# Performance work log

Hardware: AMD Instinct MI355X
Metric: run time of the kernel (lower is better)

## Reference

```python
import jax, jax.numpy as jnp
import numpy as np

N = 50000      # nodes
E = 800000     # edges (avg degree 16)
IN_DIM = 128
HID = 64       # num_hidden
HEADS = 1
NUM_LAYERS = 3       # -> 4 SNATConv layers total
SLOPE = 0.2          # negative_slope
THR = 0.01           # threhold: edges with attention < THR are pruned after layer 0


def setup_inputs() -> dict:
    key = jax.random.key(0)
    ks = jax.random.split(key, 16)
    s = 0.05
    x = jax.random.normal(ks[0], (N, IN_DIM), jnp.float32)
    edge_src = jax.random.randint(ks[1], (E,), 0, N)
    edge_dst = jax.random.randint(ks[2], (E,), 0, N)
    W_embed = jax.random.normal(ks[3], (IN_DIM, HID), jnp.float32) * s
    n_conv = NUM_LAYERS + 1
    # all conv layers map HID*HEADS -> HEADS*HID (heads==1 so square)
    W_gat = jax.random.normal(ks[4], (n_conv, HID, HEADS * HID), jnp.float32) * s
    a_l = jax.random.normal(ks[5], (n_conv, HEADS, HID), jnp.float32) * s
    a_r = jax.random.normal(ks[6], (n_conv, HEADS, HID), jnp.float32) * s
    d_cat = (NUM_LAYERS + 1) * HID
    W0 = jax.random.normal(ks[7], (d_cat, HID), jnp.float32) * s
    b0 = jnp.zeros((HID,), jnp.float32)
    W1 = jax.random.normal(ks[8], (HID, HID), jnp.float32) * s
    b1 = jnp.zeros((HID,), jnp.float32)
    W2 = jax.random.normal(ks[9], (HID, 1), jnp.float32) * s
    b2 = jnp.zeros((1,), jnp.float32)
    return {"x": x, "edge_src": edge_src, "edge_dst": edge_dst,
            "W_embed": W_embed, "W_gat": W_gat, "a_l": a_l, "a_r": a_r,
            "W0": W0, "b0": b0, "W1": W1, "b1": b1, "W2": W2, "b2": b2}


def _edge_softmax(e, dst):
    # e: [E, H] raw scores; softmax over incoming edges of each dst node
    m = jax.ops.segment_max(e, dst, num_segments=N)       # [N, H]
    a = jnp.exp(e - m[dst])
    s = jax.ops.segment_sum(a, dst, num_segments=N)       # [N, H]
    return a / jnp.maximum(s[dst], 1e-9)


def _snat_conv(h, W, al, ar, src, dst, mask):
    # h: [N, F_in]; W: [F_in, H*HID]; al/ar: [H, HID]
    feat = (h @ W).reshape(N, HEADS, HID)                 # [N, H, HID]
    el = jnp.sum(feat * al, axis=-1)                      # [N, H]
    er = jnp.sum(feat * ar, axis=-1)
    e = jax.nn.leaky_relu(el[src] + er[dst], SLOPE)       # [E, H]
    if mask is not None:
        e = jnp.where(mask, e, -1e9)                      # prune thresholded edges
    alpha = _edge_softmax(e, dst)                         # [E, H]
    out = jax.ops.segment_sum(feat[src] * alpha[..., None], dst, num_segments=N)
    return jax.nn.elu(out), alpha                         # [N, H, HID], [E, H]


def reference(x, edge_src, edge_dst, W_embed, W_gat, a_l, a_r, W0, b0, W1, b1, W2, b2):
    src, dst = edge_src, edge_dst
    h = jnp.tanh(x @ W_embed)                             # [N, HID]
    # layer 0: computes attention and the threshold mask (index_1 / index_0)
    h0, alpha = _snat_conv(h, W_gat[0], a_l[0], a_r[0], src, dst, None)
    mask = alpha >= THR                                   # [E, H] kept-edge mask
    h = h0.reshape(N, HEADS * HID)
    H_cat = [h]
    for l in range(1, NUM_LAYERS):                        # middle layers reuse mask
        hl, _ = _snat_conv(h, W_gat[l], a_l[l], a_r[l], src, dst, mask)
        h = hl.reshape(N, HEADS * HID)
        H_cat.append(h)
    feats, _ = _snat_conv(h, W_gat[NUM_LAYERS], a_l[NUM_LAYERS], a_r[NUM_LAYERS], src, dst, mask)
    feats = feats.mean(axis=1)                            # [N, HID] mean over heads
    f = jnp.concatenate(H_cat + [feats], axis=1)          # [N, (L+1)*HID]
    out = jax.nn.relu(f @ W0 + b0)                        # activationP
    out = jax.nn.relu(out @ W1 + b1)
    out = jax.nn.relu(out @ W2 + b2)                      # final F.relu
    return out                                            # [N, 1]
```

## Files before the change

### kernel.cpp

```cpp
#include <hip/hip_runtime.h>
#include <math.h>


#define CAP 80

__global__ void k_zero(int* __restrict__ counts, int N) {
  int i = blockIdx.x * 256 + threadIdx.x;
  if (i < N) counts[i] = 0;
}

__global__ void k_scatter2(const int* __restrict__ src, const int* __restrict__ dst,
                           int* __restrict__ counts, int* __restrict__ csr_src,
                           int E) {
  int e = blockIdx.x * blockDim.x + threadIdx.x;
  if (e < E) {
    int d = dst[e];
    int pos = atomicAdd(&counts[d], 1);
    if (pos < CAP) csr_src[d * CAP + pos] = src[e];
  }
}

#define SWS 68

#define STAGE_W(DST, SRC)                                            \
  {                                                                  \
    int k_ = threadIdx.x >> 2, p_ = threadIdx.x & 3;                 \
    const float* s_ = (SRC) + k_ * 64 + p_ * 16;                     \
    float* d_ = (DST) + k_ * SWS + p_ * 16;                          \
    _Pragma("unroll")                                                \
    for (int c_ = 0; c_ < 4; c_++)                                   \
      *(float4*)(d_ + c_ * 4) = *(const float4*)(s_ + c_ * 4);       \
  }

#define GEMM64(ACC, ABASE, ASTRIDE, KOFF)                            \
  { _Pragma("unroll 4")                                              \
    for (int k_ = 0; k_ < 64; k_++) {                                \
      float4 w4_ = *(const float4*)&sW[k_ * SWS + fq];               \
      float a0_ = (ABASE)[(nr +  0) * (ASTRIDE) + (KOFF) + k_];      \
      float a1_ = (ABASE)[(nr + 16) * (ASTRIDE) + (KOFF) + k_];      \
      float a2_ = (ABASE)[(nr + 32) * (ASTRIDE) + (KOFF) + k_];      \
      float a3_ = (ABASE)[(nr + 48) * (ASTRIDE) + (KOFF) + k_];      \
      ACC[0][0] = fmaf(a0_, w4_.x, ACC[0][0]);                       \
      ACC[0][1] = fmaf(a0_, w4_.y, ACC[0][1]);                       \
      ACC[0][2] = fmaf(a0_, w4_.z, ACC[0][2]);                       \
      ACC[0][3] = fmaf(a0_, w4_.w, ACC[0][3]);                       \
      ACC[1][0] = fmaf(a1_, w4_.x, ACC[1][0]);                       \
      ACC[1][1] = fmaf(a1_, w4_.y, ACC[1][1]);                       \
      ACC[1][2] = fmaf(a1_, w4_.z, ACC[1][2]);                       \
      ACC[1][3] = fmaf(a1_, w4_.w, ACC[1][3]);                       \
      ACC[2][0] = fmaf(a2_, w4_.x, ACC[2][0]);                       \
      ACC[2][1] = fmaf(a2_, w4_.y, ACC[2][1]);                       \
      ACC[2][2] = fmaf(a2_, w4_.z, ACC[2][2]);                       \
      ACC[2][3] = fmaf(a2_, w4_.w, ACC[2][3]);                       \
      ACC[3][0] = fmaf(a3_, w4_.x, ACC[3][0]);                       \
      ACC[3][1] = fmaf(a3_, w4_.y, ACC[3][1]);                       \
      ACC[3][2] = fmaf(a3_, w4_.z, ACC[3][2]);                       \
      ACC[3][3] = fmaf(a3_, w4_.w, ACC[3][3]);                       \
    } }

__global__ __launch_bounds__(256, 3) void k_embed_feat(
    const float* __restrict__ x, const float* __restrict__ We,
    const float* __restrict__ Wg, const float* __restrict__ al,
    const float* __restrict__ ar, float* __restrict__ feat,
    float* __restrict__ el, float* __restrict__ er, int N) {
  __shared__ float sA[64 * 129];
  __shared__ float sW[64 * SWS];
  __shared__ float sE[64 * 8];
  int tid = threadIdx.x, lane = tid & 63, wv = tid >> 6;
  int nb0 = blockIdx.x * 64, nl = N - 1;
  int r = tid >> 2, p = tid & 3;
  int nr = lane >> 2, fc = lane & 3;
  int fq = wv * 16 + fc * 4;
  {
    const float* gp = x + (size_t)min(nb0 + r, nl) * 128;
    #pragma unroll
    for (int half = 0; half < 2; half++) {
      const float* g = gp + half * 64 + p * 16;
      float4 v0 = *(const float4*)(g + 0), v1 = *(const float4*)(g + 4);
      float4 v2 = *(const float4*)(g + 8), v3 = *(const float4*)(g + 12);
      float* dp = &sA[r * 129 + half * 64 + p * 16];
      dp[0]=v0.x; dp[1]=v0.y; dp[2]=v0.z; dp[3]=v0.w;
      dp[4]=v1.x; dp[5]=v1.y; dp[6]=v1.z; dp[7]=v1.w;
      dp[8]=v2.x; dp[9]=v2.y; dp[10]=v2.z; dp[11]=v2.w;
      dp[12]=v3.x; dp[13]=v3.y; dp[14]=v3.z; dp[15]=v3.w;
    }
  }
  STAGE_W(sW, We);
  __syncthreads();
  float acc[4][4];
  #pragma unroll
  for (int m = 0; m < 4; m++)
    #pragma unroll
    for (int j = 0; j < 4; j++) acc[m][j] = 0.f;
  GEMM64(acc, sA, 129, 0);
  __syncthreads();
  STAGE_W(sW, We + 4096);
  __syncthreads();
  GEMM64(acc, sA, 129, 64);
  __syncthreads();
  STAGE_W(sW, Wg);
  #pragma unroll
  for (int m = 0; m < 4; m++)
    #pragma unroll
    for (int j = 0; j < 4; j++)
      sA[(nr + 16 * m) * 65 + fq + j] = tanhf(acc[m][j]);
  __syncthreads();
  float acc2[4][4];
  #pragma unroll
  for (int m = 0; m < 4; m++)
    #pragma unroll
    for (int j = 0; j < 4; j++) acc2[m][j] = 0.f;
  GEMM64(acc2, sA, 65, 0);
  {
    float alv[4], arv[4];
    *(float4*)&alv[0] = *(const float4*)(al + fq);
    *(float4*)&arv[0] = *(const float4*)(ar + fq);
    #pragma unroll
    for (int m = 0; m < 4; m++) {
      float pl = 0.f, pr = 0.f;
      #pragma unroll
      for (int j = 0; j < 4; j++) {
        pl = fmaf(acc2[m][j], alv[j], pl);
        pr = fmaf(acc2[m][j], arv[j], pr);
      }
      pl += __shfl_xor(pl, 1, 64); pl += __shfl_xor(pl, 2, 64);
      pr += __shfl_xor(pr, 1, 64); pr += __shfl_xor(pr, 2, 64);
      if (fc == 0) {
        sE[(nr + 16 * m) * 8 + wv] = pl;
        sE[(nr + 16 * m) * 8 + 4 + wv] = pr;
      }
    }
  }
  __syncthreads();
  #pragma unroll
  for (int m = 0; m < 4; m++)
    #pragma unroll
    for (int j = 0; j < 4; j++)
      sA[(nr + 16 * m) * 65 + fq + j] = acc2[m][j];
  __syncthreads();
  {
    int n = nb0 + r;
    if (n < N) {
      const float* sp = &sA[r * 65 + p * 16];
      float* gp = feat + (size_t)n * 64 + p * 16;
      #pragma unroll
      for (int q = 0; q < 4; q++)
        *(float4*)(gp + q * 4) = make_float4(sp[q*4+0], sp[q*4+1], sp[q*4+2], sp[q*4+3]);
    }
  }
  if (tid < 64) {
    int n = nb0 + tid;
    if (n < N) {
      el[n] = (sE[tid*8+0] + sE[tid*8+1]) + (sE[tid*8+2] + sE[tid*8+3]);
      er[n] = (sE[tid*8+4] + sE[tid*8+5]) + (sE[tid*8+6] + sE[tid*8+7]);
    }
  }
}

__global__ __launch_bounds__(256, 3) void k_feat(const float* __restrict__ hin,
                                                 const float* __restrict__ Wg,
                                                 const float* __restrict__ al,
                                                 const float* __restrict__ ar,
                                                 float* __restrict__ feat,
                                                 float* __restrict__ el,
                                                 float* __restrict__ er, int N) {
  __shared__ float sA[64 * 65];
  __shared__ float sW[64 * SWS];
  __shared__ float sE[64 * 8];
  int tid = threadIdx.x, lane = tid & 63, wv = tid >> 6;
  int nb0 = blockIdx.x * 64;
  int nl = N - 1;
  int r = tid >> 2, p = tid & 3;
  int nr = lane >> 2, fc = lane & 3;
  int fq = wv * 16 + fc * 4;
  {
    const float* g = hin + (size_t)min(nb0 + r, nl) * 64 + p * 16;
    float4 v0 = *(const float4*)(g + 0), v1 = *(const float4*)(g + 4);
    float4 v2 = *(const float4*)(g + 8), v3 = *(const float4*)(g + 12);
    float* dp = &sA[r * 65 + p * 16];
    dp[0]=v0.x; dp[1]=v0.y; dp[2]=v0.z; dp[3]=v0.w;
    dp[4]=v1.x; dp[5]=v1.y; dp[6]=v1.z; dp[7]=v1.w;
    dp[8]=v2.x; dp[9]=v2.y; dp[10]=v2.z; dp[11]=v2.w;
    dp[12]=v3.x; dp[13]=v3.y; dp[14]=v3.z; dp[15]=v3.w;
  }
  STAGE_W(sW, Wg);
  __syncthreads();
  float acc[4][4];
  #pragma unroll
  for (int m = 0; m < 4; m++)
    #pragma unroll
    for (int j = 0; j < 4; j++) acc[m][j] = 0.f;
  GEMM64(acc, sA, 65, 0);
  {
    float alv[4], arv[4];
    *(float4*)&alv[0] = *(const float4*)(al + fq);
    *(float4*)&arv[0] = *(const float4*)(ar + fq);
    #pragma unroll
    for (int m = 0; m < 4; m++) {
      float pl = 0.f, pr = 0.f;
      #pragma unroll
      for (int j = 0; j < 4; j++) {
        pl = fmaf(acc[m][j], alv[j], pl);
        pr = fmaf(acc[m][j], arv[j], pr);
      }
      pl += __shfl_xor(pl, 1, 64); pl += __shfl_xor(pl, 2, 64);
      pr += __shfl_xor(pr, 1, 64); pr += __shfl_xor(pr, 2, 64);
      if (fc == 0) {
        sE[(nr + 16 * m) * 8 + wv] = pl;
        sE[(nr + 16 * m) * 8 + 4 + wv] = pr;
      }
    }
  }
  __syncthreads();
  #pragma unroll
  for (int m = 0; m < 4; m++)
    #pragma unroll
    for (int j = 0; j < 4; j++)
      sA[(nr + 16 * m) * 65 + fq + j] = acc[m][j];
  __syncthreads();
  {
    int n = nb0 + r;
    if (n < N) {
      const float* sp = &sA[r * 65 + p * 16];
      float* gp = feat + (size_t)n * 64 + p * 16;
      #pragma unroll
      for (int q = 0; q < 4; q++)
        *(float4*)(gp + q * 4) = make_float4(sp[q*4+0], sp[q*4+1], sp[q*4+2], sp[q*4+3]);
    }
  }
  if (tid < 64) {
    int n = nb0 + tid;
    if (n < N) {
      el[n] = (sE[tid*8+0] + sE[tid*8+1]) + (sE[tid*8+2] + sE[tid*8+3]);
      er[n] = (sE[tid*8+4] + sE[tid*8+5]) + (sE[tid*8+6] + sE[tid*8+7]);
    }
  }
}

__global__ __launch_bounds__(256) void k_aggr(const float* __restrict__ feat,
                                              const float* __restrict__ el,
                                              const float* __restrict__ er,
                                              const int* __restrict__ counts,
                                              const int* __restrict__ csr_src,
                                              unsigned char* __restrict__ mask,
                                              int write_mask, int use_mask,
                                              float* __restrict__ hout, int N) {
  __shared__ __align__(16) int   su[4][64];
  __shared__ __align__(16) float spl[4][64];
  int wv = (int)((blockIdx.x * blockDim.x + threadIdx.x) >> 6);
  int wave = threadIdx.x >> 6, lane = threadIdx.x & 63;
  if (wv >= N) return;
  int beg = wv * CAP;
  int deg = min(counts[wv], CAP);
  int end = beg + deg;
  float erv = er[wv];
  float acc0 = 0.f, acc1 = 0.f, acc2 = 0.f, acc3 = 0.f;
  if (deg <= 64) {
    int k = beg + lane;
    bool have = (lane < deg);
    int u = have ? csr_src[k] : 0;
    float sc = -INFINITY;
    if (have) {
      float e0 = el[u] + erv;
      sc = (e0 >= 0.f) ? e0 : 0.2f * e0;
      if (use_mask && mask[k] == 0) sc = -1e9f;
    }
    float m = sc;
    #pragma unroll
    for (int off = 32; off; off >>= 1) m = fmaxf(m, __shfl_xor(m, off, 64));
    float pl = have ? expf(sc - m) : 0.f;
    float s = pl;
    #pragma unroll
    for (int off = 32; off; off >>= 1) s += __shfl_xor(s, off, 64);
    pl *= 1.0f / fmaxf(s, 1e-9f);
    if (write_mask && have) mask[k] = (pl >= 0.01f) ? 1 : 0;
    su[wave][lane] = u;
    spl[wave][lane] = pl;
    int dq = (deg + 3) >> 2;
    #pragma unroll 2
    for (int q = 0; q < dq; q++) {
      int4   uu = *(const int4*)&su[wave][q * 4];
      float4 pp = *(const float4*)&spl[wave][q * 4];
      acc0 = fmaf(pp.x, feat[(size_t)uu.x * 64 + lane], acc0);
      acc1 = fmaf(pp.y, feat[(size_t)uu.y * 64 + lane], acc1);
      acc2 = fmaf(pp.z, feat[(size_t)uu.z * 64 + lane], acc2);
      acc3 = fmaf(pp.w, feat[(size_t)uu.w * 64 + lane], acc3);
    }
  } else {
    float m = -INFINITY, s = 0.f;
    for (int base = beg; base < end; base += 64) {
      int k = base + lane;
      float sc = -INFINITY;
      if (k < end) {
        int u = csr_src[k];
        float e0 = el[u] + erv;
        sc = (e0 >= 0.f) ? e0 : 0.2f * e0;
        if (use_mask && mask[k] == 0) sc = -1e9f;
      }
      float cm = sc;
      #pragma unroll
      for (int off = 32; off; off >>= 1) cm = fmaxf(cm, __shfl_xor(cm, off, 64));
      float nm = fmaxf(m, cm);
      float t = (k < end) ? expf(sc - nm) : 0.f;
      #pragma unroll
      for (int off = 32; off; off >>= 1) t += __shfl_xor(t, off, 64);
      s = s * expf(m - nm) + t;
      m = nm;
    }
    float inv = 1.0f / fmaxf(s, 1e-9f);
    for (int base = beg; base < end; base += 64) {
      int k = base + lane;
      int u = 0;
      float pl = 0.f;
      if (k < end) {
        u = csr_src[k];
        float e0 = el[u] + erv;
        float sc = (e0 >= 0.f) ? e0 : 0.2f * e0;
        if (use_mask && mask[k] == 0) sc = -1e9f;
        pl = expf(sc - m) * inv;
        if (write_mask) mask[k] = (pl >= 0.01f) ? 1 : 0;
      }
      su[wave][lane] = u;
      spl[wave][lane] = pl;
      int cnt = min(64, end - base);
      int dq = (cnt + 3) >> 2;
      for (int q = 0; q < dq; q++) {
        int4   uu = *(const int4*)&su[wave][q * 4];
        float4 pp = *(const float4*)&spl[wave][q * 4];
        acc0 = fmaf(pp.x, feat[(size_t)uu.x * 64 + lane], acc0);
        acc1 = fmaf(pp.y, feat[(size_t)uu.y * 64 + lane], acc1);
        acc2 = fmaf(pp.z, feat[(size_t)uu.z * 64 + lane], acc2);
        acc3 = fmaf(pp.w, feat[(size_t)uu.w * 64 + lane], acc3);
      }
    }
  }
  float acc = (acc0 + acc1) + (acc2 + acc3);
  hout[(size_t)wv * 64 + lane] = (acc > 0.f) ? acc : expm1f(acc);
}

__global__ __launch_bounds__(256, 3) void k_mlp(const float* __restrict__ o0,
                                                const float* __restrict__ o1,
                                                const float* __restrict__ o2,
                                                const float* __restrict__ o3,
                                                const float* __restrict__ W0,
                                                const float* __restrict__ b0,
                                                const float* __restrict__ W1,
                                                const float* __restrict__ b1,
                                                const float* __restrict__ W2,
                                                const float* __restrict__ b2,
                                                float* __restrict__ out, int N) {
  __shared__ float sA[64 * 65];
  __shared__ float sW[64 * SWS];
  __shared__ float sR[64 * 5];
  int tid = threadIdx.x, lane = tid & 63, wv = tid >> 6;
  int nb0 = blockIdx.x * 64;
  int nl = N - 1;
  int r = tid >> 2, p = tid & 3;
  int nr = lane >> 2, fc = lane & 3;
  int fq = wv * 16 + fc * 4;
  float acc[4][4];
  {
    float4 b0v = *(const float4*)(b0 + fq);
    #pragma unroll
    for (int m = 0; m < 4; m++) {
      acc[m][0] = b0v.x; acc[m][1] = b0v.y;
      acc[m][2] = b0v.z; acc[m][3] = b0v.w;
    }
  }

  auto seg = [&](const float* __restrict__ sp, const float* __restrict__ wp) {
    __syncthreads();
    {
      const float* g = sp + (size_t)min(nb0 + r, nl) * 64 + p * 16;
      float4 v0 = *(const float4*)(g + 0), v1 = *(const float4*)(g + 4);
      float4 v2 = *(const float4*)(g + 8), v3 = *(const float4*)(g + 12);
      float* dp = &sA[r * 65 + p * 16];
      dp[0]=v0.x; dp[1]=v0.y; dp[2]=v0.z; dp[3]=v0.w;
      dp[4]=v1.x; dp[5]=v1.y; dp[6]=v1.z; dp[7]=v1.w;
      dp[8]=v2.x; dp[9]=v2.y; dp[10]=v2.z; dp[11]=v2.w;
      dp[12]=v3.x; dp[13]=v3.y; dp[14]=v3.z; dp[15]=v3.w;
    }
    STAGE_W(sW, wp);
    __syncthreads();
    GEMM64(acc, sA, 65, 0);
  };
  seg(o0, W0);
  seg(o1, W0 + 64 * 64);
  seg(o2, W0 + 128 * 64);
  seg(o3, W0 + 192 * 64);

  __syncthreads();
  STAGE_W(sW, W1);
  #pragma unroll
  for (int m = 0; m < 4; m++)
    #pragma unroll
    for (int j = 0; j < 4; j++) {
      float z = acc[m][j];
      sA[(nr + 16 * m) * 65 + fq + j] = (z > 0.f) ? z : 0.f;
    }
  __syncthreads();
  float a1[4][4];
  {
    float4 b1v = *(const float4*)(b1 + fq);
    #pragma unroll
    for (int m = 0; m < 4; m++) {
      a1[m][0] = b1v.x; a1[m][1] = b1v.y;
      a1[m][2] = b1v.z; a1[m][3] = b1v.w;
    }
  }
  GEMM64(a1, sA, 65, 0);
  {
    float4 w2v = *(const float4*)(W2 + fq);
    float w2a[4] = {w2v.x, w2v.y, w2v.z, w2v.w};
    #pragma unroll
    for (int m = 0; m < 4; m++) {
      float rp = 0.f;
      #pragma unroll
      for (int j = 0; j < 4; j++) {
        float t = (a1[m][j] > 0.f) ? a1[m][j] : 0.f;
        rp = fmaf(t, w2a[j], rp);
      }
      rp += __shfl_xor(rp, 1, 64); rp += __shfl_xor(rp, 2, 64);
      if (fc == 0) sR[(nr + 16 * m) * 5 + wv] = rp;
    }
  }
  __syncthreads();
  if (tid < 64) {
    int n = nb0 + tid;
    if (n < N) {
      float o = (sR[tid*5+0] + sR[tid*5+1]) + (sR[tid*5+2] + sR[tid*5+3]) + b2[0];
      out[n] = (o > 0.f) ? o : 0.f;
    }
  }
}

extern "C" void kernel_launch(void* const* d_in, const int* in_sizes, int n_in,
                              void* d_out, int out_size, void* d_ws, size_t ws_size,
                              hipStream_t stream) {
  const float* x       = (const float*)d_in[0];
  const int*   esrc    = (const int*)d_in[1];
  const int*   edst    = (const int*)d_in[2];
  const float* W_embed = (const float*)d_in[3];
  const float* W_gat   = (const float*)d_in[4];
  const float* a_l     = (const float*)d_in[5];
  const float* a_r     = (const float*)d_in[6];
  const float* W0      = (const float*)d_in[7];
  const float* b0      = (const float*)d_in[8];
  const float* W1      = (const float*)d_in[9];
  const float* b1      = (const float*)d_in[10];
  const float* W2      = (const float*)d_in[11];
  const float* b2      = (const float*)d_in[12];
  float* out = (float*)d_out;
  const int N = in_sizes[0] / 128;
  const int E = in_sizes[1];

  char* p = (char*)d_ws;
  auto alloc = [&](size_t bytes) -> char* {
    char* r = p;
    p += (bytes + 255) & ~(size_t)255;
    return r;
  };
  float* out0 = (float*)alloc((size_t)N * 64 * 4);
  float* out1 = (float*)alloc((size_t)N * 64 * 4);
  float* out2 = (float*)alloc((size_t)N * 64 * 4);
  float* out3 = (float*)alloc((size_t)N * 64 * 4);
  float* feat = (float*)alloc((size_t)N * 64 * 4);
  float* el   = (float*)alloc((size_t)N * 4);
  float* er   = (float*)alloc((size_t)N * 4);
  int* counts  = (int*)alloc((size_t)N * 4);
  int* csr_src = (int*)alloc((size_t)N * CAP * 4);
  unsigned char* mask = (unsigned char*)alloc((size_t)N * CAP);

  k_zero<<<(N + 255) / 256, 256, 0, stream>>>(counts, N);
  k_scatter2<<<(E + 255) / 256, 256, 0, stream>>>(esrc, edst, counts, csr_src, E);

  int dgb = (N + 63) / 64;

  k_embed_feat<<<dgb, 256, 0, stream>>>(x, W_embed, W_gat,
                                        a_l, a_r, feat, el, er, N);
  float* outs[4] = {out0, out1, out2, out3};
  k_aggr<<<(N + 3) / 4, 256, 0, stream>>>(feat, el, er, counts, csr_src, mask,
                                          1, 0, out0, N);

  for (int l = 1; l < 4; l++) {
    k_feat<<<dgb, 256, 0, stream>>>(outs[l - 1], W_gat + (size_t)l * 4096,
                                    a_l + (size_t)l * 64, a_r + (size_t)l * 64,
                                    feat, el, er, N);
    k_aggr<<<(N + 3) / 4, 256, 0, stream>>>(feat, el, er, counts, csr_src, mask,
                                            0, 1, outs[l], N);
  }

  k_mlp<<<dgb, 256, 0, stream>>>(out0, out1, out2, out3, W0, b0,
                                 W1, b1, W2, b2, out, N);
}
```

Before: 406.2 us.

## Fuse edge CSR scatter into embed/feature kernel via interleaved block roles

Removes the separate edge-scatter kernel and assigns odd blocks of the embedding+feature kernel to build the CSR adjacency with atomics, while even blocks do the node GEMM work. Each scatter thread now handles four edges using int4 loads. The goal is to save a kernel launch and overlap the atomic-heavy scatter with compute-bound GEMM blocks. The cost is that scatter blocks still reserve the large shared memory footprint of the GEMM path, which may limit occupancy, and the grid is sized by the larger of the two work counts.

Result: faster. 378.8 us (-6.8%).

```diff
diff --git a/kernel.cpp b/kernel.cpp
--- a/kernel.cpp
+++ b/kernel.cpp
@@ -7,17 +7,6 @@
 __global__ void k_zero(int* __restrict__ counts, int N) {
   int i = blockIdx.x * 256 + threadIdx.x;
   if (i < N) counts[i] = 0;
-}
-
-__global__ void k_scatter2(const int* __restrict__ src, const int* __restrict__ dst,
-                           int* __restrict__ counts, int* __restrict__ csr_src,
-                           int E) {
-  int e = blockIdx.x * blockDim.x + threadIdx.x;
-  if (e < E) {
-    int d = dst[e];
-    int pos = atomicAdd(&counts[d], 1);
-    if (pos < CAP) csr_src[d * CAP + pos] = src[e];
-  }
 }
 
 #define SWS 68
@@ -58,16 +47,40 @@
       ACC[3][3] = fmaf(a3_, w4_.w, ACC[3][3]);                       \
     } }
 
-__global__ __launch_bounds__(256, 3) void k_embed_feat(
+__global__ __launch_bounds__(256, 3) void k_front(
     const float* __restrict__ x, const float* __restrict__ We,
     const float* __restrict__ Wg, const float* __restrict__ al,
     const float* __restrict__ ar, float* __restrict__ feat,
-    float* __restrict__ el, float* __restrict__ er, int N) {
+    float* __restrict__ el, float* __restrict__ er, int N,
+    const int* __restrict__ esrc, const int* __restrict__ edst,
+    int* __restrict__ counts, int* __restrict__ csr_src, int E) {
   __shared__ float sA[64 * 129];
   __shared__ float sW[64 * SWS];
   __shared__ float sE[64 * 8];
+  int bid = blockIdx.x;
+  if (bid & 1) {
+    int base = (bid >> 1) * 1024 + threadIdx.x * 4;
+    if (base + 3 < E) {
+      int4 s4 = *(const int4*)(esrc + base);
+      int4 d4 = *(const int4*)(edst + base);
+      int s[4] = {s4.x, s4.y, s4.z, s4.w};
+      int d[4] = {d4.x, d4.y, d4.z, d4.w};
+      #pragma unroll
+      for (int i = 0; i < 4; i++) {
+        int pos = atomicAdd(&counts[d[i]], 1);
+        if (pos < CAP) csr_src[d[i] * CAP + pos] = s[i];
+      }
+    } else {
+      for (int i = 0; i < 4 && base + i < E; i++) {
+        int dv = edst[base + i];
+        int pos = atomicAdd(&counts[dv], 1);
+        if (pos < CAP) csr_src[dv * CAP + pos] = esrc[base + i];
+      }
+    }
+    return;
+  }
   int tid = threadIdx.x, lane = tid & 63, wv = tid >> 6;
-  int nb0 = blockIdx.x * 64, nl = N - 1;
+  int nb0 = (bid >> 1) * 64, nl = N - 1;
   int r = tid >> 2, p = tid & 3;
   int nr = lane >> 2, fc = lane & 3;
   int fq = wv * 16 + fc * 4;
@@ -472,12 +485,14 @@
   unsigned char* mask = (unsigned char*)alloc((size_t)N * CAP);
 
   k_zero<<<(N + 255) / 256, 256, 0, stream>>>(counts, N);
-  k_scatter2<<<(E + 255) / 256, 256, 0, stream>>>(esrc, edst, counts, csr_src, E);
 
   int dgb = (N + 63) / 64;
-
-  k_embed_feat<<<dgb, 256, 0, stream>>>(x, W_embed, W_gat,
-                                        a_l, a_r, feat, el, er, N);
+  int sgb = (E + 1023) / 1024;
+  int fgb = 2 * ((dgb > sgb) ? dgb : sgb);
+
+  k_front<<<fgb, 256, 0, stream>>>(x, W_embed, W_gat, a_l, a_r,
+                                   feat, el, er, N,
+                                   esrc, edst, counts, csr_src, E);
   float* outs[4] = {out0, out1, out2, out3};
   k_aggr<<<(N + 3) / 4, 256, 0, stream>>>(feat, el, er, counts, csr_src, mask,
                                           1, 0, out0, N);
```
